# Kernel optimization log

Measured on AMD Instinct MI355X. Metric: run time of the kernel, lower is better.

Reference implementation:

```python
import jax, jax.numpy as jnp
import numpy as np

B, C, H, W_ = 16, 512, 32, 32
NH = 8
DK = C // NH  # 64


def setup_inputs() -> dict:
    key = jax.random.key(0)
    ks = jax.random.split(key, 7)
    s = 1.0 / np.sqrt(C).astype(np.float32)
    x = jax.random.normal(ks[0], (B, C, H, W_), jnp.float32)
    # 1x1 convs == per-pixel channel matmuls; weight shape (out_c, in_c)
    w_q = jax.random.normal(ks[1], (C, C), jnp.float32) * s
    w_k = jax.random.normal(ks[2], (C, C), jnp.float32) * s
    w_v = jax.random.normal(ks[3], (C, C), jnp.float32) * s
    w_o = jax.random.normal(ks[4], (C, C), jnp.float32) * s
    b_o = jnp.zeros((C,), jnp.float32)
    ps = DK ** -0.5
    rel_h = jax.random.normal(ks[5], (2 * H - 1, DK), jnp.float32) * ps
    rel_w = jax.random.normal(ks[6], (2 * W_ - 1, DK), jnp.float32) * ps
    return dict(x=x, w_q=w_q, w_k=w_k, w_v=w_v, w_o=w_o, b_o=b_o,
                rel_h=rel_h, rel_w=rel_w)


def _rel_pos_bias(q, rel_h, rel_w):
    # q: (B, NH, H*W, DK). Content-aware 2D relative position bias:
    # bias[x,y,i,j] = q[x,y]·rel_w[j-y+W-1] + q[x,y]·rel_h[i-x+H-1]
    q4 = q.reshape(B, NH, H, W_, DK)
    idx_w = jnp.arange(W_)[None, :] - jnp.arange(W_)[:, None] + (W_ - 1)  # (Wq,Wk)
    idx_h = jnp.arange(H)[None, :] - jnp.arange(H)[:, None] + (H - 1)     # (Hq,Hk)
    lw = jnp.einsum('bnxyd,rd->bnxyr', q4, rel_w)                # (B,NH,H,W,2W-1)
    aw = jnp.take_along_axis(lw, idx_w[None, None, None], axis=-1)  # (B,NH,H,Wq,Wk)
    lh = jnp.einsum('bnxyd,rd->bnxyr', q4, rel_h)                # (B,NH,H,W,2H-1)
    ah = jnp.take_along_axis(lh.swapaxes(2, 3), idx_h[None, None, None], axis=-1)
    ah = ah.swapaxes(2, 3)                                       # (B,NH,Hq,Wq,Hk)
    bias = ah[..., :, None] + aw[..., None, :]                   # (B,NH,H,W,Hk,Wk)
    return bias.reshape(B, NH, H * W_, H * W_)


def reference(x, w_q, w_k, w_v, w_o, b_o, rel_h, rel_w):
    def proj(w):
        y = jnp.einsum('oc,bchw->bohw', w, x)
        # rearrange 'b (dk h) hi wi -> b h (hi wi) dk' (d_k outer, head inner)
        return y.reshape(B, DK, NH, H * W_).transpose(0, 2, 3, 1)

    q = proj(w_q)  # (B,NH,N,DK), N = H*W
    k = proj(w_k)
    v = proj(w_v)

    energy = jnp.einsum('bnqd,bnkd->bnqk', q, k)
    bias = _rel_pos_bias(q, rel_h, rel_w)
    scores = jax.nn.softmax((energy + bias) / np.sqrt(DK).astype(np.float32), axis=-1)
    out = jnp.einsum('bnqk,bnkd->bnqd', scores, v)
    # rearrange 'b h (hi wi) d -> b (h d) hi wi' (head outer, d_k inner)
    out = out.transpose(0, 1, 3, 2).reshape(B, C, H, W_)
    out = jnp.einsum('oc,bchw->bohw', w_o, out) + b_o[None, :, None, None]
    return out
```

## Files before the change

kernel.cpp:

```cpp
#include <hip/hip_runtime.h>

typedef __attribute__((ext_vector_type(8))) short s8v;
typedef __attribute__((ext_vector_type(4))) float f4v;
typedef __attribute__((ext_vector_type(4))) unsigned short u4v;
typedef __attribute__((ext_vector_type(2))) unsigned int u2v;
typedef __attribute__((ext_vector_type(4))) float fl4;

#define MFMA __builtin_amdgcn_mfma_f32_16x16x32_bf16
#define LOG2E 1.44269504088896340736f
#define QSCALE (0.125f * LOG2E)

__device__ __forceinline__ unsigned short f2bf(float f) {
  return (unsigned short)((__float_as_uint(f) + 0x8000u) >> 16);
}
__device__ __forceinline__ unsigned int pack_bf(float a, float b) {
  return __builtin_amdgcn_perm(__float_as_uint(b) + 0x8000u,
                               __float_as_uint(a) + 0x8000u, 0x07060302u);
}
__device__ __forceinline__ float bf2f(unsigned short u) {
  return __uint_as_float(((unsigned int)u) << 16);
}

__device__ __forceinline__ void gload16(const void* g, void* l) {
  __builtin_amdgcn_global_load_lds(
      (const __attribute__((address_space(1))) unsigned int*)g,
      (__attribute__((address_space(3))) unsigned int*)l,
      16, 0, 0);
}

__device__ __forceinline__ void stage64(unsigned short* lds,
                                        const unsigned short* src,
                                        int src_ld, int tid) {
  const int w = tid >> 6, l = tid & 63;
#pragma unroll
  for (int c = 0; c < 2; ++c) {
    int idx = (c * 4 + w) * 64 + l;
    int row = idx >> 3, cl = idx & 7;
    gload16(src + row * src_ld + ((cl ^ (row & 7)) << 3),
            lds + (c * 4 + w) * 512);
  }
}
__device__ __forceinline__ void stage64_8w(unsigned short* lds,
                                           const unsigned short* src,
                                           int src_ld, int w, int l) {
  int row = w * 8 + (l >> 3), cl = l & 7;
  gload16(src + row * src_ld + ((cl ^ (row & 7)) << 3),
          lds + w * 512);
}
__device__ __forceinline__ void stage128(unsigned short* lds,
                                         const unsigned short* src,
                                         int src_ld, int tid) {
  const int w = tid >> 6, l = tid & 63;
#pragma unroll
  for (int c = 0; c < 4; ++c) {
    int id = c * 256 + w * 64 + l;
    int row = id >> 3, cl = id & 7;
    gload16(src + row * src_ld + ((cl ^ (row & 7)) << 3),
            lds + (c * 256 + w * 64) * 8);
  }
}
__device__ __forceinline__ s8v frag64(const unsigned short* lds, int row, int chunk) {
  return *(const s8v*)(lds + row * 64 + ((chunk ^ (row & 7)) << 3));
}

__global__ void cvt_all(const float* __restrict__ wq, const float* __restrict__ wk,
                        const float* __restrict__ wv, const float* __restrict__ wo,
                        const float* __restrict__ relh, const float* __restrict__ relw,
                        unsigned short* __restrict__ Wqkv, unsigned short* __restrict__ Wob,
                        unsigned short* __restrict__ Rel) {
  const int bid = blockIdx.x, tid = threadIdx.x;
  if (bid < 768) {
    int i = bid * 256 + tid;
    int orow = i >> 7, c4 = (i & 127) * 4;
    int p = orow >> 9, oc = orow & 511;
    int h = oc >> 6, d = oc & 63;
    const float* w = (p == 0) ? wq : (p == 1) ? wk : wv;
    fl4 v = *(const fl4*)(w + (d * 8 + h) * 512 + c4);
    u4v o;
    o[0] = f2bf(v[0]); o[1] = f2bf(v[1]); o[2] = f2bf(v[2]); o[3] = f2bf(v[3]);
    *(u4v*)(Wqkv + orow * 512 + c4) = o;
  } else if (bid < 1024) {
    int i = (bid - 768) * 256 + tid;
    fl4 v = ((const fl4*)wo)[i];
    u4v o;
    o[0] = f2bf(v[0]); o[1] = f2bf(v[1]); o[2] = f2bf(v[2]); o[3] = f2bf(v[3]);
    ((u4v*)Wob)[i] = o;
  } else {
    int i = (bid - 1024) * 256 + tid;
    int t = i >> 12, r = (i >> 6) & 63, d = i & 63;
    const float* s = t ? relw : relh;
    Rel[i] = (r < 63) ? f2bf(s[r * 64 + d]) : (unsigned short)0;
  }
}

__global__ void xpose(const float* __restrict__ x, unsigned short* __restrict__ Xt) {
  __shared__ float tls[32][33];
  const int c0 = blockIdx.x * 32, n0 = blockIdx.y * 32, b = blockIdx.z;
  const int tid = threadIdx.x;
  const int rr = tid >> 3, cc4 = (tid & 7) * 4;
  fl4 v = *(const fl4*)(x + (b * 512 + c0 + rr) * 1024 + n0 + cc4);
#pragma unroll
  for (int i = 0; i < 4; ++i) tls[rr][cc4 + i] = v[i];
  __syncthreads();
  u4v o;
#pragma unroll
  for (int i = 0; i < 4; ++i) o[i] = f2bf(tls[cc4 + i][rr]);
  *(u4v*)(Xt + (b * 1024 + n0 + rr) * 512 + c0 + cc4) = o;
}

__global__ __launch_bounds__(256, 2)
void qkv_gemm(const unsigned short* __restrict__ W,
              const unsigned short* __restrict__ Xt,
              unsigned short* __restrict__ qb,
              unsigned short* __restrict__ kb,
              unsigned short* __restrict__ vtb) {
  __shared__ __align__(16) unsigned short Al[8192];
  __shared__ __align__(16) unsigned short Bl[8192];
  const int tid = threadIdx.x, w = tid >> 6, l = tid & 63;
  const int l15 = l & 15, lg = l >> 4;
  const int wr = w >> 1, wc = w & 1;
  const int bid = blockIdx.x;
  const int cls = bid & 7, idx = bid >> 3;
  const int n0 = cls * 128;
  const int m0 = (idx % 12) * 128;
  const int b  = idx / 12;
  f4v acc[4][4] = {};
  const unsigned short* As = W + m0 * 512;
  const unsigned short* Bs = Xt + (b * 1024 + n0) * 512;
  for (int k0 = 0; k0 < 512; k0 += 64) {
    stage128(Al, As + k0, 512, tid);
    stage128(Bl, Bs + k0, 512, tid);
    __syncthreads();
#pragma unroll
    for (int kk = 0; kk < 2; ++kk) {
      s8v a[4], bb[4];
#pragma unroll
      for (int i = 0; i < 4; ++i) a[i] = frag64(Al + wr * 4096, i * 16 + l15, kk * 4 + lg);
#pragma unroll
      for (int j = 0; j < 4; ++j) bb[j] = frag64(Bl + wc * 4096, j * 16 + l15, kk * 4 + lg);
#pragma unroll
      for (int i = 0; i < 4; ++i)
#pragma unroll
        for (int j = 0; j < 4; ++j)
          acc[i][j] = MFMA(a[i], bb[j], acc[i][j], 0, 0, 0);
    }
    __syncthreads();
  }
  const int p = m0 >> 9;
  const float sc = (p == 0) ? QSCALE : 1.0f;
#pragma unroll
  for (int i = 0; i < 4; ++i) {
    int o = m0 + wr * 64 + i * 16 + lg * 4;
    int oc = o & 511, hh = oc >> 6, dd = oc & 63;
#pragma unroll
    for (int j = 0; j < 4; ++j) {
      int n = n0 + wc * 64 + j * 16 + l15;
      if (p < 2) {
        u2v pk;
        pk[0] = pack_bf(acc[i][j][0] * sc, acc[i][j][1] * sc);
        pk[1] = pack_bf(acc[i][j][2] * sc, acc[i][j][3] * sc);
        unsigned short* dst = (p == 0 ? qb : kb) + (((b * 8 + hh) * 1024 + n) * 64 + dd);
        *(u2v*)dst = pk;
      } else {
#pragma unroll
        for (int r = 0; r < 4; ++r)
          vtb[((b * 8 + hh) * 64 + dd + r) * 1024 + n] = f2bf(acc[i][j][r]);
      }
    }
  }
}

__global__ __launch_bounds__(512, 4)
void attn_kernel(const unsigned short* __restrict__ qbuf,
                 const unsigned short* __restrict__ kbuf,
                 const unsigned short* __restrict__ vtbuf,
                 const unsigned short* __restrict__ relb,
                 unsigned short* __restrict__ AO) {
  __shared__ __align__(16) unsigned short SH[34304];
  unsigned short* K0  = SH;
  unsigned short* V0  = SH + 4096;
  unsigned short* K1  = SH + 8192;
  unsigned short* V1  = SH + 12288;
  unsigned short* lhb = SH + 16384;
  unsigned short* PwB = SH + 25088;

  const int tid = threadIdx.x, w = tid >> 6, l = tid & 63;
  const int l15 = l & 15, lg = l >> 4;
  const int bid = blockIdx.x;
  const int cls = bid & 7, idx = bid >> 3;
  const int q0 = (idx & 7) * 128;
  const int bh = cls + 8 * (idx >> 3);
  const unsigned short* qh = qbuf + bh * 65536;
  const unsigned short* kh = kbuf + bh * 65536;
  const unsigned short* vh = vtbuf + bh * 65536;
  const int qloc = w * 16 + l15;
  const int qrow = q0 + qloc;
  const int x = qrow >> 5, y = qrow & 31;

  stage64_8w(K0, kh, 64, w, l);
  stage64_8w(V0, vh, 1024, w, l);

  s8v bq[2];
#pragma unroll
  for (int kk = 0; kk < 2; ++kk)
    bq[kk] = *(const s8v*)(qh + qrow * 64 + kk * 32 + lg * 8);

#pragma unroll
  for (int ct = 0; ct < 4; ++ct) {
    f4v c = {0.f, 0.f, 0.f, 0.f};
#pragma unroll
    for (int kk = 0; kk < 2; ++kk) {
      s8v a = *(const s8v*)(relb + 4096 + (ct * 16 + l15) * 64 + kk * 32 + lg * 8);
      c = MFMA(a, bq[kk], c, 0, 0, 0);
    }
    u2v pk;
    pk[0] = pack_bf(c[0], c[1]);
    pk[1] = pack_bf(c[2], c[3]);
    *(u2v*)(lhb + qloc * 68 + ct * 16 + lg * 4) = pk;
  }
  float lwreg[2][4];
#pragma unroll
  for (int c1 = 0; c1 < 2; ++c1)
#pragma unroll
    for (int r = 0; r < 4; ++r)
      lwreg[c1][r] = bf2f(lhb[qloc * 68 + (c1 * 16 + lg * 4 + r) - y + 31]);
#pragma unroll
  for (int ct = 0; ct < 4; ++ct) {
    f4v c = {0.f, 0.f, 0.f, 0.f};
#pragma unroll
    for (int kk = 0; kk < 2; ++kk) {
      s8v a = *(const s8v*)(relb + (ct * 16 + l15) * 64 + kk * 32 + lg * 8);
      c = MFMA(a, bq[kk], c, 0, 0, 0);
    }
    u2v pk;
    pk[0] = pack_bf(c[0], c[1]);
    pk[1] = pack_bf(c[2], c[3]);
    *(u2v*)(lhb + qloc * 68 + ct * 16 + lg * 4) = pk;
  }

  float lsum = 0.f;
  f4v ao[4] = {};
  unsigned short* pw = PwB + w * 1152;

  auto tile = [&](const unsigned short* Kc, const unsigned short* Vc, int n0) {
    int ib = qloc * 68 + (n0 >> 5) - x + 31;
    float lh0 = bf2f(lhb[ib]);
    float lh1 = bf2f(lhb[ib + 1]);
#pragma unroll
    for (int ct = 0; ct < 4; ++ct) {
      float lh = (ct & 2) ? lh1 : lh0;
      f4v c;
#pragma unroll
      for (int r = 0; r < 4; ++r) c[r] = lh + lwreg[ct & 1][r];
#pragma unroll
      for (int kk = 0; kk < 2; ++kk)
        c = MFMA(frag64(Kc, ct * 16 + l15, kk * 4 + lg), bq[kk], c, 0, 0, 0);
      f4v e;
#pragma unroll
      for (int r = 0; r < 4; ++r) e[r] = __builtin_amdgcn_exp2f(c[r]);
      lsum += (e[0] + e[1]) + (e[2] + e[3]);
      u2v pk;
      pk[0] = pack_bf(e[0], e[1]);
      pk[1] = pack_bf(e[2], e[3]);
      *(u2v*)(pw + l15 * 72 + ct * 16 + lg * 4) = pk;
    }
    s8v ap[2];
#pragma unroll
    for (int kk = 0; kk < 2; ++kk)
      ap[kk] = *(const s8v*)(pw + l15 * 72 + kk * 32 + lg * 8);
#pragma unroll
    for (int dt = 0; dt < 4; ++dt)
#pragma unroll
      for (int kk = 0; kk < 2; ++kk)
        ao[dt] = MFMA(frag64(Vc, dt * 16 + l15, kk * 4 + lg), ap[kk], ao[dt], 0, 0, 0);
  };

  __syncthreads();
  for (int t = 0; t < 16; t += 2) {
    stage64_8w(K1, kh + (t + 1) * 4096, 64, w, l);
    stage64_8w(V1, vh + (t + 1) * 64, 1024, w, l);
    tile(K0, V0, t * 64);
    __syncthreads();
    if (t < 14) {
      stage64_8w(K0, kh + (t + 2) * 4096, 64, w, l);
      stage64_8w(V0, vh + (t + 2) * 64, 1024, w, l);
    }
    tile(K1, V1, (t + 1) * 64);
    __syncthreads();
  }

  lsum += __shfl_xor(lsum, 16);
  lsum += __shfl_xor(lsum, 32);
  float inv = 1.0f / lsum;
#pragma unroll
  for (int dt = 0; dt < 4; ++dt) {
    u2v pk;
    pk[0] = pack_bf(ao[dt][0] * inv, ao[dt][1] * inv);
    pk[1] = pack_bf(ao[dt][2] * inv, ao[dt][3] * inv);
    *(u2v*)(AO + (bh * 1024 + qrow) * 64 + dt * 16 + lg * 4) = pk;
  }
}

__global__ __launch_bounds__(256, 2)
void out_gemm(const unsigned short* __restrict__ Wo,
              const unsigned short* __restrict__ AO,
              const float* __restrict__ bo,
              float* __restrict__ out) {
  __shared__ __align__(16) unsigned short Al[8192];
  __shared__ __align__(16) unsigned short Bl[8192];
  const int tid = threadIdx.x, w = tid >> 6, l = tid & 63;
  const int l15 = l & 15, lg = l >> 4;
  const int wr = w >> 1, wc = w & 1;
  const int bid = blockIdx.x;
  const int cls = bid & 7, idx = bid >> 3;
  const int n0 = cls * 128;
  const int m0 = (idx & 3) * 128;
  const int b  = idx >> 2;
  f4v acc[4][4] = {};
  for (int k0 = 0; k0 < 512; k0 += 64) {
    stage128(Al, Wo + m0 * 512 + k0, 512, tid);
    stage128(Bl, AO + ((b * 8 + (k0 >> 6)) * 1024 + n0) * 64, 64, tid);
    __syncthreads();
#pragma unroll
    for (int kk = 0; kk < 2; ++kk) {
      s8v a[4], bb[4];
#pragma unroll
      for (int i = 0; i < 4; ++i) a[i] = frag64(Al + wr * 4096, i * 16 + l15, kk * 4 + lg);
#pragma unroll
      for (int j = 0; j < 4; ++j) bb[j] = frag64(Bl + wc * 4096, j * 16 + l15, kk * 4 + lg);
#pragma unroll
      for (int i = 0; i < 4; ++i)
#pragma unroll
        for (int j = 0; j < 4; ++j)
          acc[i][j] = MFMA(a[i], bb[j], acc[i][j], 0, 0, 0);
    }
    __syncthreads();
  }
#pragma unroll
  for (int i = 0; i < 4; ++i) {
    int ob = m0 + wr * 64 + i * 16 + lg * 4;
    float b0 = bo[ob], b1 = bo[ob + 1], b2 = bo[ob + 2], b3 = bo[ob + 3];
#pragma unroll
    for (int j = 0; j < 4; ++j) {
      int n = n0 + wc * 64 + j * 16 + l15;
      float* op = out + (b * 512 + ob) * 1024 + n;
      op[0]    = acc[i][j][0] + b0;
      op[1024] = acc[i][j][1] + b1;
      op[2048] = acc[i][j][2] + b2;
      op[3072] = acc[i][j][3] + b3;
    }
  }
}


extern "C" void kernel_launch(void* const* d_in, const int* in_sizes, int n_in,
                              void* d_out, int out_size, void* d_ws, size_t ws_size,
                              hipStream_t stream) {
  const float* x    = (const float*)d_in[0];
  const float* wq   = (const float*)d_in[1];
  const float* wk   = (const float*)d_in[2];
  const float* wv   = (const float*)d_in[3];
  const float* wo   = (const float*)d_in[4];
  const float* bo   = (const float*)d_in[5];
  const float* relh = (const float*)d_in[6];
  const float* relw = (const float*)d_in[7];
  char* ws = (char*)d_ws;
  unsigned short* Xt   = (unsigned short*)(ws + 0);
  unsigned short* AO   = (unsigned short*)(ws + 0);
  unsigned short* Wqkv = (unsigned short*)(ws + 16777216);
  unsigned short* Wob  = (unsigned short*)(ws + 18350080);
  unsigned short* Rel  = (unsigned short*)(ws + 18874368);
  unsigned short* Qb   = (unsigned short*)(ws + 18890752);
  unsigned short* Kb   = (unsigned short*)(ws + 35667968);
  unsigned short* Vt   = (unsigned short*)(ws + 52445184);
  float* out = (float*)d_out;

  cvt_all<<<1056, 256, 0, stream>>>(wq, wk, wv, wo, relh, relw, Wqkv, Wob, Rel);
  xpose<<<dim3(16, 32, 16), 256, 0, stream>>>(x, Xt);
  qkv_gemm<<<1536, 256, 0, stream>>>(Wqkv, Xt, Qb, Kb, Vt);
  attn_kernel<<<1024, 512, 0, stream>>>(Qb, Kb, Vt, Rel, AO);
  out_gemm<<<512, 256, 0, stream>>>(Wob, AO, bo, out);
}
```

Measured before the change: 202.5 us.

## Single-buffer attention K/V tiles to raise occupancy; merge prep kernels

The attention kernel drops its double-buffered K/V staging and uses one LDS buffer. This shrinks shared memory from about 67KB to about 51KB per block and raises the launch-bounds occupancy hint from 4 to 6. The trade-off is that loads no longer overlap compute within a block: each tile now waits behind two barriers for its load. Separately, the weight-conversion and x-transpose kernels are fused into one launch to save a kernel launch.

```diff
diff --git a/kernel.cpp b/kernel.cpp
--- a/kernel.cpp
+++ b/kernel.cpp
@@ -28,18 +28,6 @@
       16, 0, 0);
 }
 
-__device__ __forceinline__ void stage64(unsigned short* lds,
-                                        const unsigned short* src,
-                                        int src_ld, int tid) {
-  const int w = tid >> 6, l = tid & 63;
-#pragma unroll
-  for (int c = 0; c < 2; ++c) {
-    int idx = (c * 4 + w) * 64 + l;
-    int row = idx >> 3, cl = idx & 7;
-    gload16(src + row * src_ld + ((cl ^ (row & 7)) << 3),
-            lds + (c * 4 + w) * 512);
-  }
-}
 __device__ __forceinline__ void stage64_8w(unsigned short* lds,
                                            const unsigned short* src,
                                            int src_ld, int w, int l) {
@@ -63,49 +51,50 @@
   return *(const s8v*)(lds + row * 64 + ((chunk ^ (row & 7)) << 3));
 }
 
-__global__ void cvt_all(const float* __restrict__ wq, const float* __restrict__ wk,
-                        const float* __restrict__ wv, const float* __restrict__ wo,
-                        const float* __restrict__ relh, const float* __restrict__ relw,
-                        unsigned short* __restrict__ Wqkv, unsigned short* __restrict__ Wob,
-                        unsigned short* __restrict__ Rel) {
+__global__ void prep(const float* __restrict__ x,
+                     const float* __restrict__ wq, const float* __restrict__ wk,
+                     const float* __restrict__ wv, const float* __restrict__ wo,
+                     const float* __restrict__ relh, const float* __restrict__ relw,
+                     unsigned short* __restrict__ Xt, unsigned short* __restrict__ Wqkv,
+                     unsigned short* __restrict__ Wob, unsigned short* __restrict__ Rel) {
+  __shared__ float tls[32][33];
   const int bid = blockIdx.x, tid = threadIdx.x;
-  if (bid < 768) {
-    int i = bid * 256 + tid;
-    int orow = i >> 7, c4 = (i & 127) * 4;
-    int p = orow >> 9, oc = orow & 511;
-    int h = oc >> 6, d = oc & 63;
-    const float* w = (p == 0) ? wq : (p == 1) ? wk : wv;
-    fl4 v = *(const fl4*)(w + (d * 8 + h) * 512 + c4);
+  if (bid < 8192) {
+    const int c0 = (bid & 15) * 32, n0 = ((bid >> 4) & 31) * 32, b = bid >> 9;
+    const int rr = tid >> 3, cc4 = (tid & 7) * 4;
+    fl4 v = *(const fl4*)(x + (b * 512 + c0 + rr) * 1024 + n0 + cc4);
+#pragma unroll
+    for (int i = 0; i < 4; ++i) tls[rr][cc4 + i] = v[i];
+    __syncthreads();
     u4v o;
-    o[0] = f2bf(v[0]); o[1] = f2bf(v[1]); o[2] = f2bf(v[2]); o[3] = f2bf(v[3]);
-    *(u4v*)(Wqkv + orow * 512 + c4) = o;
-  } else if (bid < 1024) {
-    int i = (bid - 768) * 256 + tid;
-    fl4 v = ((const fl4*)wo)[i];
-    u4v o;
-    o[0] = f2bf(v[0]); o[1] = f2bf(v[1]); o[2] = f2bf(v[2]); o[3] = f2bf(v[3]);
-    ((u4v*)Wob)[i] = o;
+#pragma unroll
+    for (int i = 0; i < 4; ++i) o[i] = f2bf(tls[cc4 + i][rr]);
+    *(u4v*)(Xt + (b * 1024 + n0 + rr) * 512 + c0 + cc4) = o;
   } else {
-    int i = (bid - 1024) * 256 + tid;
-    int t = i >> 12, r = (i >> 6) & 63, d = i & 63;
-    const float* s = t ? relw : relh;
-    Rel[i] = (r < 63) ? f2bf(s[r * 64 + d]) : (unsigned short)0;
-  }
-}
-
-__global__ void xpose(const float* __restrict__ x, unsigned short* __restrict__ Xt) {
-  __shared__ float tls[32][33];
-  const int c0 = blockIdx.x * 32, n0 = blockIdx.y * 32, b = blockIdx.z;
-  const int tid = threadIdx.x;
-  const int rr = tid >> 3, cc4 = (tid & 7) * 4;
-  fl4 v = *(const fl4*)(x + (b * 512 + c0 + rr) * 1024 + n0 + cc4);
-#pragma unroll
-  for (int i = 0; i < 4; ++i) tls[rr][cc4 + i] = v[i];
-  __syncthreads();
-  u4v o;
-#pragma unroll
-  for (int i = 0; i < 4; ++i) o[i] = f2bf(tls[cc4 + i][rr]);
-  *(u4v*)(Xt + (b * 1024 + n0 + rr) * 512 + c0 + cc4) = o;
+    const int cb = bid - 8192;
+    if (cb < 768) {
+      int i = cb * 256 + tid;
+      int orow = i >> 7, c4 = (i & 127) * 4;
+      int p = orow >> 9, oc = orow & 511;
+      int h = oc >> 6, d = oc & 63;
+      const float* w = (p == 0) ? wq : (p == 1) ? wk : wv;
+      fl4 v = *(const fl4*)(w + (d * 8 + h) * 512 + c4);
+      u4v o;
+      o[0] = f2bf(v[0]); o[1] = f2bf(v[1]); o[2] = f2bf(v[2]); o[3] = f2bf(v[3]);
+      *(u4v*)(Wqkv + orow * 512 + c4) = o;
+    } else if (cb < 1024) {
+      int i = (cb - 768) * 256 + tid;
+      fl4 v = ((const fl4*)wo)[i];
+      u4v o;
+      o[0] = f2bf(v[0]); o[1] = f2bf(v[1]); o[2] = f2bf(v[2]); o[3] = f2bf(v[3]);
+      ((u4v*)Wob)[i] = o;
+    } else {
+      int i = (cb - 1024) * 256 + tid;
+      int t = i >> 12, r = (i >> 6) & 63, d = i & 63;
+      const float* s = t ? relw : relh;
+      Rel[i] = (r < 63) ? f2bf(s[r * 64 + d]) : (unsigned short)0;
+    }
+  }
 }
 
 __global__ __launch_bounds__(256, 2)
@@ -170,19 +159,17 @@
   }
 }
 
-__global__ __launch_bounds__(512, 4)
+__global__ __launch_bounds__(512, 6)
 void attn_kernel(const unsigned short* __restrict__ qbuf,
                  const unsigned short* __restrict__ kbuf,
                  const unsigned short* __restrict__ vtbuf,
                  const unsigned short* __restrict__ relb,
                  unsigned short* __restrict__ AO) {
-  __shared__ __align__(16) unsigned short SH[34304];
-  unsigned short* K0  = SH;
-  unsigned short* V0  = SH + 4096;
-  unsigned short* K1  = SH + 8192;
-  unsigned short* V1  = SH + 12288;
-  unsigned short* lhb = SH + 16384;
-  unsigned short* PwB = SH + 25088;
+  __shared__ __align__(16) unsigned short SH[26112];
+  unsigned short* Kl  = SH;
+  unsigned short* Vl  = SH + 4096;
+  unsigned short* lhb = SH + 8192;
+  unsigned short* PwB = SH + 16896;
 
   const int tid = threadIdx.x, w = tid >> 6, l = tid & 63;
   const int l15 = l & 15, lg = l >> 4;
@@ -197,8 +184,8 @@
   const int qrow = q0 + qloc;
   const int x = qrow >> 5, y = qrow & 31;
 
-  stage64_8w(K0, kh, 64, w, l);
-  stage64_8w(V0, vh, 1024, w, l);
+  stage64_8w(Kl, kh, 64, w, l);
+  stage64_8w(Vl, vh, 1024, w, l);
 
   s8v bq[2];
 #pragma unroll
@@ -242,7 +229,7 @@
   f4v ao[4] = {};
   unsigned short* pw = PwB + w * 1152;
 
-  auto tile = [&](const unsigned short* Kc, const unsigned short* Vc, int n0) {
+  auto tile = [&](int n0) {
     int ib = qloc * 68 + (n0 >> 5) - x + 31;
     float lh0 = bf2f(lhb[ib]);
     float lh1 = bf2f(lhb[ib + 1]);
@@ -254,7 +241,7 @@
       for (int r = 0; r < 4; ++r) c[r] = lh + lwreg[ct & 1][r];
 #pragma unroll
       for (int kk = 0; kk < 2; ++kk)
-        c = MFMA(frag64(Kc, ct * 16 + l15, kk * 4 + lg), bq[kk], c, 0, 0, 0);
+        c = MFMA(frag64(Kl, ct * 16 + l15, kk * 4 + lg), bq[kk], c, 0, 0, 0);
       f4v e;
 #pragma unroll
       for (int r = 0; r < 4; ++r) e[r] = __builtin_amdgcn_exp2f(c[r]);
@@ -272,21 +259,18 @@
     for (int dt = 0; dt < 4; ++dt)
 #pragma unroll
       for (int kk = 0; kk < 2; ++kk)
-        ao[dt] = MFMA(frag64(Vc, dt * 16 + l15, kk * 4 + lg), ap[kk], ao[dt], 0, 0, 0);
+        ao[dt] = MFMA(frag64(Vl, dt * 16 + l15, kk * 4 + lg), ap[kk], ao[dt], 0, 0, 0);
   };
 
   __syncthreads();
-  for (int t = 0; t < 16; t += 2) {
-    stage64_8w(K1, kh + (t + 1) * 4096, 64, w, l);
-    stage64_8w(V1, vh + (t + 1) * 64, 1024, w, l);
-    tile(K0, V0, t * 64);
-    __syncthreads();
-    if (t < 14) {
-      stage64_8w(K0, kh + (t + 2) * 4096, 64, w, l);
-      stage64_8w(V0, vh + (t + 2) * 64, 1024, w, l);
-    }
-    tile(K1, V1, (t + 1) * 64);
-    __syncthreads();
+  for (int t = 0; t < 16; ++t) {
+    tile(t * 64);
+    if (t < 15) {
+      __syncthreads();
+      stage64_8w(Kl, kh + (t + 1) * 4096, 64, w, l);
+      stage64_8w(Vl, vh + (t + 1) * 64, 1024, w, l);
+      __syncthreads();
+    }
   }
 
   lsum += __shfl_xor(lsum, 16);
@@ -375,8 +359,7 @@
   unsigned short* Vt   = (unsigned short*)(ws + 52445184);
   float* out = (float*)d_out;
 
-  cvt_all<<<1056, 256, 0, stream>>>(wq, wk, wv, wo, relh, relw, Wqkv, Wob, Rel);
-  xpose<<<dim3(16, 32, 16), 256, 0, stream>>>(x, Xt);
+  prep<<<9248, 256, 0, stream>>>(x, wq, wk, wv, wo, relh, relw, Xt, Wqkv, Wob, Rel);
   qkv_gemm<<<1536, 256, 0, stream>>>(Wqkv, Xt, Qb, Kb, Vt);
   attn_kernel<<<1024, 512, 0, stream>>>(Qb, Kb, Vt, Rel, AO);
   out_gemm<<<512, 256, 0, stream>>>(Wob, AO, bo, out);
```

Result: slower. 217.8 us (+7.6%).
